# Kernel tuning notes

Hardware: AMD Instinct MI355X
Metric: run time of the kernel (lower is better)

Reference implementation:

```python
import jax, jax.numpy as jnp
import numpy as np

B, T, I, E, K, J = 4, 4096, 512, 16, 1024, 512

def setup_inputs() -> dict:
    key = jax.random.key(0)
    k1, k2, k3 = jax.random.split(key, 3)
    X = jax.random.normal(k1, (B, T, I), dtype=jnp.float32)
    ind = jax.random.randint(k2, (B, E, K), 0, T, dtype=jnp.int64)
    W = jax.random.normal(k3, (E, I, J), dtype=jnp.float32)
    return {"X": X, "ind": ind, "W": W}

def reference(X, ind, W):
    # X: [B,T,I], ind: [B,E,K] indices into T (per batch), W: [E,I,J]
    b, t, i = X.shape
    offset = (jnp.arange(b, dtype=ind.dtype) * t)[:, None, None]  # [B,1,1]
    X_flat = X.reshape(b * t, i)
    gathered = X_flat[ind + offset]              # [B,E,K,I]
    Y = jnp.einsum('beki,eij->bekj', gathered, W)  # [B,E,K,J]
    return Y
```

## Files before the change

### kernel.cpp

```cpp
#include <hip/hip_runtime.h>

#define B_ 4
#define T_ 4096
#define I_ 512
#define E_ 16
#define K_ 1024
#define J_ 512

typedef unsigned short u16;
typedef __attribute__((ext_vector_type(4))) float floatx4;
typedef __attribute__((ext_vector_type(8))) short short8;
typedef __attribute__((ext_vector_type(4))) unsigned int uintx4;
typedef __attribute__((ext_vector_type(4))) u16 u16x4;
typedef __attribute__((ext_vector_type(8))) u16 u16x8;

__device__ __forceinline__ u16 f2bf(float f) {
  unsigned int u = __float_as_uint(f);
  u += 0x7FFFu + ((u >> 16) & 1u);
  return (u16)(u >> 16);
}

__global__ __launch_bounds__(256) void cvt_x(const float* __restrict__ X,
                                             u16* __restrict__ Xb) {
  const int n4 = B_ * T_ * I_ / 4;
  int i = blockIdx.x * 256 + threadIdx.x;
  const int stride = gridDim.x * 256;
  for (; i < n4; i += stride) {
    floatx4 v = ((const floatx4*)X)[i];
    u16x4 o;
    o[0] = f2bf(v[0]); o[1] = f2bf(v[1]); o[2] = f2bf(v[2]); o[3] = f2bf(v[3]);
    ((u16x4*)Xb)[i] = o;
  }
}

__global__ __launch_bounds__(256) void transp_w(const float* __restrict__ W,
                                                u16* __restrict__ Wt) {
  __shared__ u16 tile[64][65];
  const int tid = threadIdx.x;
  const int blk = blockIdx.x;
  const int e  = blk >> 6;
  const int bi = (blk >> 3) & 7;
  const int bj = blk & 7;
  const int i0 = bi * 64, j0 = bj * 64;

#pragma unroll
  for (int p = 0; p < 4; ++p) {
    int r = p * 16 + (tid >> 4);
    int c = (tid & 15) * 4;
    floatx4 v = *(const floatx4*)(W + ((size_t)(e * I_ + i0 + r)) * J_ + j0 + c);
    tile[r][c + 0] = f2bf(v[0]);
    tile[r][c + 1] = f2bf(v[1]);
    tile[r][c + 2] = f2bf(v[2]);
    tile[r][c + 3] = f2bf(v[3]);
  }
  __syncthreads();
#pragma unroll
  for (int p = 0; p < 2; ++p) {
    int j = p * 32 + (tid >> 3);
    int ch = tid & 7;
    u16x8 o;
#pragma unroll
    for (int s = 0; s < 8; ++s) o[s] = tile[ch * 8 + s][j];
    *(u16x8*)(Wt + ((size_t)(e * J_ + j0 + j)) * I_ + i0 + ch * 8) = o;
  }
}

__global__ __launch_bounds__(256) void gemm_gather(const u16* __restrict__ Xb,
                                                   const u16* __restrict__ Wt,
                                                   const int* __restrict__ ind,
                                                   float* __restrict__ Y) {
  __shared__ alignas(16) u16 As[128][72];
  __shared__ alignas(16) u16 Bs[128][72];

  const int tid = threadIdx.x;
  const int blk = blockIdx.x;
  const int n_t = blk & 3;
  const int m_t = (blk >> 2) & 7;
  const int be  = blk >> 5;
  const int e = be & 15;
  const int b = be >> 4;

  const int ch = tid & 7;
  const int rb = tid >> 3;

  const u16* aptr[4];
  const u16* bptr[4];
#pragma unroll
  for (int p = 0; p < 4; ++p) {
    const int r = p * 32 + rb;
    const int t = ind[be * K_ + m_t * 128 + r];
    aptr[p] = Xb + ((size_t)(b * T_ + t)) * I_ + ch * 8;
    bptr[p] = Wt + ((size_t)(e * J_ + n_t * 128 + r)) * I_ + ch * 8;
  }

  const int lane = tid & 63;
  const int wave = tid >> 6;
  const int wm = (wave >> 1) * 64;
  const int wn = (wave & 1) * 64;
  const int ml = lane & 15;
  const int quad = lane >> 4;

  floatx4 acc[4][4] = {};

  for (int kk = 0; kk < I_; kk += 64) {
#pragma unroll
    for (int p = 0; p < 4; ++p) {
      const int r = p * 32 + rb;
      *(uintx4*)&As[r][ch * 8] = *(const uintx4*)(aptr[p] + kk);
      *(uintx4*)&Bs[r][ch * 8] = *(const uintx4*)(bptr[p] + kk);
    }
    __syncthreads();
#pragma unroll
    for (int s = 0; s < 2; ++s) {
      short8 af[4], bf[4];
#pragma unroll
      for (int i = 0; i < 4; ++i) {
        af[i] = *(const short8*)&As[wm + i * 16 + ml][s * 32 + quad * 8];
        bf[i] = *(const short8*)&Bs[wn + i * 16 + ml][s * 32 + quad * 8];
      }
#pragma unroll
      for (int i = 0; i < 4; ++i)
#pragma unroll
        for (int j = 0; j < 4; ++j)
          acc[i][j] = __builtin_amdgcn_mfma_f32_16x16x32_bf16(
              af[i], bf[j], acc[i][j], 0, 0, 0);
    }
    __syncthreads();
  }

#pragma unroll
  for (int i = 0; i < 4; ++i) {
    const int row0 = m_t * 128 + wm + i * 16 + quad * 4;
#pragma unroll
    for (int j = 0; j < 4; ++j) {
      const int col = n_t * 128 + wn + j * 16 + ml;
      float* yp = Y + ((size_t)(be * K_ + row0)) * J_ + col;
#pragma unroll
      for (int r = 0; r < 4; ++r) yp[(size_t)r * J_] = acc[i][j][r];
    }
  }
}

extern "C" void kernel_launch(void* const* d_in, const int* in_sizes, int n_in,
                              void* d_out, int out_size, void* d_ws,
                              size_t ws_size, hipStream_t stream) {
  const float* X  = (const float*)d_in[0];
  const int* ind  = (const int*)d_in[1];
  const float* W  = (const float*)d_in[2];
  float* Y = (float*)d_out;

  u16* Xb = (u16*)d_ws;
  u16* Wt = (u16*)((char*)d_ws + (size_t)B_ * T_ * I_ * 2);

  cvt_x<<<2048, 256, 0, stream>>>(X, Xb);
  transp_w<<<1024, 256, 0, stream>>>(W, Wt);
  gemm_gather<<<2048, 256, 0, stream>>>(Xb, Wt, ind, Y);
}
```

Baseline: 216.6 us.

## Load GEMM tiles via direct global-to-LDS with XOR swizzle and vectorized stores

Replaces register-staged global loads into padded shared tiles with global_load_lds direct-to-LDS transfers into an unpadded layout. An XOR swizzle on the 16-byte column group avoids bank conflicts without padding. The MFMA operands are swapped so each lane holds four consecutive J outputs, which allows 16-byte vector stores of Y instead of scalar strided stores. This cuts VGPR pressure and the number of load/store instructions, but it relies on the builtin's per-wave contiguous LDS destination semantics being correct.

```diff
diff --git a/kernel.cpp b/kernel.cpp
--- a/kernel.cpp
+++ b/kernel.cpp
@@ -10,7 +10,6 @@
 typedef unsigned short u16;
 typedef __attribute__((ext_vector_type(4))) float floatx4;
 typedef __attribute__((ext_vector_type(8))) short short8;
-typedef __attribute__((ext_vector_type(4))) unsigned int uintx4;
 typedef __attribute__((ext_vector_type(4))) u16 u16x4;
 typedef __attribute__((ext_vector_type(8))) u16 u16x8;
 
@@ -18,6 +17,13 @@
   unsigned int u = __float_as_uint(f);
   u += 0x7FFFu + ((u >> 16) & 1u);
   return (u16)(u >> 16);
+}
+
+__device__ __forceinline__ void gload16(const u16* g, u16* l) {
+  __builtin_amdgcn_global_load_lds(
+      (const __attribute__((address_space(1))) unsigned int*)(g),
+      (__attribute__((address_space(3))) unsigned int*)(l),
+      16, 0, 0);
 }
 
 __global__ __launch_bounds__(256) void cvt_x(const float* __restrict__ X,
@@ -69,8 +75,8 @@
                                                    const u16* __restrict__ Wt,
                                                    const int* __restrict__ ind,
                                                    float* __restrict__ Y) {
-  __shared__ alignas(16) u16 As[128][72];
-  __shared__ alignas(16) u16 Bs[128][72];
+  __shared__ alignas(16) u16 Asf[128 * 64];
+  __shared__ alignas(16) u16 Bsf[128 * 64];
 
   const int tid = threadIdx.x;
   const int blk = blockIdx.x;
@@ -80,23 +86,28 @@
   const int e = be & 15;
   const int b = be >> 4;
 
-  const int ch = tid & 7;
-  const int rb = tid >> 3;
+  const int lane = tid & 63;
+  const int wave = tid >> 6;
 
-  const u16* aptr[4];
-  const u16* bptr[4];
+  const int lr = lane >> 3;
+  const int cg = (lane & 7) ^ lr;
+
+  const u16* agp[4];
+  const u16* bgp[4];
+  u16* aldst[4];
+  u16* bldst[4];
 #pragma unroll
-  for (int p = 0; p < 4; ++p) {
-    const int r = p * 32 + rb;
+  for (int q = 0; q < 4; ++q) {
+    const int r = wave * 32 + q * 8 + lr;
     const int t = ind[be * K_ + m_t * 128 + r];
-    aptr[p] = Xb + ((size_t)(b * T_ + t)) * I_ + ch * 8;
-    bptr[p] = Wt + ((size_t)(e * J_ + n_t * 128 + r)) * I_ + ch * 8;
+    agp[q] = Xb + ((size_t)(b * T_ + t)) * I_ + cg * 8;
+    bgp[q] = Wt + ((size_t)(e * J_ + n_t * 128 + r)) * I_ + cg * 8;
+    aldst[q] = Asf + (wave * 32 + q * 8) * 64;
+    bldst[q] = Bsf + (wave * 32 + q * 8) * 64;
   }
 
-  const int lane = tid & 63;
-  const int wave = tid >> 6;
-  const int wm = (wave >> 1) * 64;
-  const int wn = (wave & 1) * 64;
+  const int wj = (wave & 1) * 64;
+  const int wk = (wave >> 1) * 64;
   const int ml = lane & 15;
   const int quad = lane >> 4;
 
@@ -104,39 +115,38 @@
 
   for (int kk = 0; kk < I_; kk += 64) {
 #pragma unroll
-    for (int p = 0; p < 4; ++p) {
-      const int r = p * 32 + rb;
-      *(uintx4*)&As[r][ch * 8] = *(const uintx4*)(aptr[p] + kk);
-      *(uintx4*)&Bs[r][ch * 8] = *(const uintx4*)(bptr[p] + kk);
-    }
+    for (int q = 0; q < 4; ++q) gload16(agp[q] + kk, aldst[q]);
+#pragma unroll
+    for (int q = 0; q < 4; ++q) gload16(bgp[q] + kk, bldst[q]);
     __syncthreads();
 #pragma unroll
     for (int s = 0; s < 2; ++s) {
-      short8 af[4], bf[4];
+      short8 wf[4], xf[4];
+      const int c = s * 4 + quad;
 #pragma unroll
       for (int i = 0; i < 4; ++i) {
-        af[i] = *(const short8*)&As[wm + i * 16 + ml][s * 32 + quad * 8];
-        bf[i] = *(const short8*)&Bs[wn + i * 16 + ml][s * 32 + quad * 8];
+        const int jr = wj + i * 16 + ml;
+        const int kr = wk + i * 16 + ml;
+        wf[i] = *(const short8*)&Bsf[jr * 64 + ((c ^ (jr & 7)) * 8)];
+        xf[i] = *(const short8*)&Asf[kr * 64 + ((c ^ (kr & 7)) * 8)];
       }
 #pragma unroll
-      for (int i = 0; i < 4; ++i)
+      for (int iw = 0; iw < 4; ++iw)
 #pragma unroll
-        for (int j = 0; j < 4; ++j)
-          acc[i][j] = __builtin_amdgcn_mfma_f32_16x16x32_bf16(
-              af[i], bf[j], acc[i][j], 0, 0, 0);
+        for (int ik = 0; ik < 4; ++ik)
+          acc[iw][ik] = __builtin_amdgcn_mfma_f32_16x16x32_bf16(
+              wf[iw], xf[ik], acc[iw][ik], 0, 0, 0);
     }
     __syncthreads();
   }
 
 #pragma unroll
-  for (int i = 0; i < 4; ++i) {
-    const int row0 = m_t * 128 + wm + i * 16 + quad * 4;
+  for (int iw = 0; iw < 4; ++iw) {
+    const int j0 = n_t * 128 + wj + iw * 16 + quad * 4;
 #pragma unroll
-    for (int j = 0; j < 4; ++j) {
-      const int col = n_t * 128 + wn + j * 16 + ml;
-      float* yp = Y + ((size_t)(be * K_ + row0)) * J_ + col;
-#pragma unroll
-      for (int r = 0; r < 4; ++r) yp[(size_t)r * J_] = acc[i][j][r];
+    for (int ik = 0; ik < 4; ++ik) {
+      const int k0 = m_t * 128 + wk + ik * 16 + ml;
+      *(floatx4*)(Y + ((size_t)(be * K_ + k0)) * J_ + j0) = acc[iw][ik];
     }
   }
 }
```

Result: no change. 215.5 us (-0.5%).
